# Optimization experiments

Hardware: AMD Instinct MI355X
Metric: run time of the kernel (lower is better)

## Reference

```python
import jax, jax.numpy as jnp
import numpy as np

H = 512; W = 512; WL = 8; SS = 4; DIM = 128; HEADS = 4; HD = DIM // HEADS; HID = 512
N = WL * WL                      # tokens per window = 64
NW = (H // WL) * (W // WL)       # num windows = 4096
EPS = 1e-5


def _rel_pos_index():
    # standard Swin relative position index for a WLxWL window
    coords = np.stack(np.meshgrid(np.arange(WL), np.arange(WL), indexing='ij')).reshape(2, -1)  # [2, N]
    rel = (coords[:, :, None] - coords[:, None, :]).transpose(1, 2, 0)  # [N, N, 2]
    rel[..., 0] += WL - 1
    rel[..., 1] += WL - 1
    rel[..., 0] *= 2 * WL - 1
    return jnp.asarray(rel.sum(-1))  # [N, N] in [0, (2WL-1)^2)


def _shift_attn_mask():
    # region ids 0/1/2 along each axis per the h_slices/w_slices loop, cnt = 3*h_id + w_id
    ids = np.zeros(H)
    ids[H - WL:H - SS] = 1
    ids[H - SS:] = 2
    img = 3.0 * ids[:, None] + ids[None, :]                     # [H, W]
    wnd = img.reshape(H // WL, WL, W // WL, WL).transpose(0, 2, 1, 3).reshape(NW, N)
    diff = wnd[:, None, :] - wnd[:, :, None]                    # [NW, N, N]
    return jnp.asarray(np.where(diff != 0, -100.0, 0.0).astype(np.float32))


REL_IDX = _rel_pos_index()
ATTN_MASK = _shift_attn_mask()


def _layernorm(v, w, b):
    mu = v.mean(-1, keepdims=True)
    var = v.var(-1, keepdims=True)
    return (v - mu) * jax.lax.rsqrt(var + EPS) * w + b


def setup_inputs() -> dict:
    key = jax.random.key(0)
    ks = jax.random.split(key, 10)
    s = 0.02
    return {
        'x': jax.random.normal(ks[0], (H * W, DIM), dtype=jnp.float32),
        'ln1_w': jnp.ones((DIM,), jnp.float32), 'ln1_b': jnp.zeros((DIM,), jnp.float32),
        'qkv_w': jax.random.normal(ks[1], (3 * DIM, DIM), jnp.float32) * s,
        'qkv_b': jnp.zeros((3 * DIM,), jnp.float32),
        'rel_bias': jax.random.normal(ks[2], ((2 * WL - 1) ** 2, HEADS), jnp.float32) * s,
        'proj_w': jax.random.normal(ks[3], (DIM, DIM), jnp.float32) * s,
        'proj_b': jnp.zeros((DIM,), jnp.float32),
        'ln2_w': jnp.ones((DIM,), jnp.float32), 'ln2_b': jnp.zeros((DIM,), jnp.float32),
        'mlp_w1': jax.random.normal(ks[4], (HID, DIM), jnp.float32) * s,
        'mlp_b1': jnp.zeros((HID,), jnp.float32),
        'mlp_w2': jax.random.normal(ks[5], (DIM, HID), jnp.float32) * s,
        'mlp_b2': jnp.zeros((DIM,), jnp.float32),
    }


def reference(x, ln1_w, ln1_b, qkv_w, qkv_b, rel_bias, proj_w, proj_b,
              ln2_w, ln2_b, mlp_w1, mlp_b1, mlp_w2, mlp_b2):
    skip = x
    xn = _layernorm(x, ln1_w, ln1_b).reshape(H, W, DIM)
    # cyclic shift
    xs = jnp.roll(xn, shift=(-SS, -SS), axis=(0, 1))
    # window partition -> [NW, N, DIM]
    xw = xs.reshape(H // WL, WL, W // WL, WL, DIM).transpose(0, 2, 1, 3, 4).reshape(NW, N, DIM)
    # qkv projection, split heads
    qkv = (xw @ qkv_w.T + qkv_b).reshape(NW, N, 3, HEADS, HD)
    q, k, v = qkv[:, :, 0], qkv[:, :, 1], qkv[:, :, 2]   # each [NW, N, HEADS, HD]
    scale = HD ** -0.5
    scores = jnp.einsum('wnhd,wmhd->whnm', q, k) * scale   # [NW, HEADS, N, N]
    bias = rel_bias[REL_IDX].transpose(2, 0, 1)            # [HEADS, N, N]
    scores = scores + bias[None] + ATTN_MASK[:, None]
    attn = jax.nn.softmax(scores, axis=-1)
    out = jnp.einsum('whnm,wmhd->wnhd', attn, v).reshape(NW, N, DIM)
    out = out @ proj_w.T + proj_b
    # window reverse
    xr = out.reshape(H // WL, W // WL, WL, WL, DIM).transpose(0, 2, 1, 3, 4).reshape(H, W, DIM)
    # reverse cyclic shift
    xr = jnp.roll(xr, shift=(SS, SS), axis=(0, 1)).reshape(H * W, DIM)
    x1 = skip + xr
    # FFN block
    h = _layernorm(x1, ln2_w, ln2_b)
    h = jax.nn.gelu(h @ mlp_w1.T + mlp_b1) @ mlp_w2.T + mlp_b2
    return x1 + h
```

## Files before the change

kernel.cpp:

```cpp
#include <hip/hip_runtime.h>
#include <hip/hip_bf16.h>


typedef __bf16 bf16x8 __attribute__((ext_vector_type(8)));
typedef __bf16 bf16x2 __attribute__((ext_vector_type(2)));
typedef float f32x4 __attribute__((ext_vector_type(4)));

#define MFMA16(a, b, c) __builtin_amdgcn_mfma_f32_16x16x32_bf16(a, b, c, 0, 0, 0)

#define SS 4
#define XS 136
#define QKS 40
#define PSS 72

#define QKV_W_OFF 0
#define PROJ_W_OFF 98304
#define W1_OFF 131072
#define W2_OFF 262144
#define BIAS_OFF 393216

__device__ __forceinline__ int regid(int u) { return (u >= 508) ? 2 : ((u >= 504) ? 1 : 0); }

__global__ __launch_bounds__(256) void prep_kernel(
    const float* __restrict__ qkv_w, const float* __restrict__ proj_w,
    const float* __restrict__ w1, const float* __restrict__ w2,
    const float* __restrict__ rel_bias, unsigned char* __restrict__ ws) {
  int tid = blockIdx.x * 256 + threadIdx.x;
  __bf16* qw = (__bf16*)(ws + QKV_W_OFF);
  __bf16* pw = (__bf16*)(ws + PROJ_W_OFF);
  __bf16* w1b = (__bf16*)(ws + W1_OFF);
  __bf16* w2b = (__bf16*)(ws + W2_OFF);
  float* btbl = (float*)(ws + BIAS_OFF);
  if (tid < 49152) {
    int e = tid & 7, lane = (tid >> 3) & 63, kk = (tid >> 9) & 3;
    int f = tid >> 11;
    int h = f / 6, nt = f % 6;
    int j = (nt >> 1) * 128 + h * 32 + (nt & 1) * 16 + (lane & 15);
    int k = kk * 32 + (lane >> 4) * 8 + e;
    qw[tid] = (__bf16)qkv_w[j * 128 + k];
  }
  if (tid < 16384) {
    int e = tid & 7, lane = (tid >> 3) & 63, kk = (tid >> 9) & 3;
    int nt2 = (tid >> 11) & 1, wid = (tid >> 12) & 3;
    int j = wid * 32 + nt2 * 16 + (lane & 15);
    int k = kk * 32 + (lane >> 4) * 8 + e;
    pw[tid] = (__bf16)proj_w[j * 128 + k];
  }
  if (tid < 65536) {
    { int e = tid & 7, lane = (tid >> 3) & 63, kk = (tid >> 9) & 3;
      int nt = (tid >> 11) & 3, wid = (tid >> 13) & 7;
      int j = wid * 64 + nt * 16 + (lane & 15);
      int k = kk * 32 + (lane >> 4) * 8 + e;
      w1b[tid] = (__bf16)w1[j * 128 + k]; }
    { int e = tid & 7, lane = (tid >> 3) & 63, kk = (tid >> 9) & 15, wid = (tid >> 13) & 7;
      int j = wid * 16 + (lane & 15);
      int k = kk * 32 + (lane >> 4) * 8 + e;
      w2b[tid] = (__bf16)w2[j * 512 + k]; }
  }
  if (tid < 16384) {
    int i = tid & 3, lane = (tid >> 2) & 63;
    int kt = (tid >> 8) & 3, qt = (tid >> 10) & 3, h = (tid >> 12) & 3;
    int n = qt * 16 + (lane & 15);
    int m = kt * 16 + (lane >> 4) * 4 + i;
    int idx = ((n >> 3) - (m >> 3) + 7) * 15 + ((n & 7) - (m & 7) + 7);
    btbl[tid] = rel_bias[idx * 4 + h];
  }
}

__global__ __launch_bounds__(256, 2) void attn_kernel(
    const float* __restrict__ x, const float* __restrict__ ln1_w, const float* __restrict__ ln1_b,
    const float* __restrict__ qkv_b, const float* __restrict__ proj_b,
    const unsigned char* __restrict__ ws, float* __restrict__ out) {
  __shared__ __attribute__((aligned(16))) __bf16 xn[64 * XS];
  __shared__ __attribute__((aligned(16))) __bf16 wreg[4][5120];
  __shared__ __attribute__((aligned(16))) __bf16 vt[4][32 * PSS];
  __shared__ __attribute__((aligned(16))) int rid[64];

  const int w = blockIdx.x;
  const int wi = w >> 6, wj = w & 63;
  const int tid = threadIdx.x;
  const int wid = tid >> 6, lane = tid & 63;
  const int lr = lane & 15, lk = lane >> 4;
  const bool edge = (wi == 63) || (wj == 63);
  const f32x4 zero4 = {0.f, 0.f, 0.f, 0.f};

  const __bf16* qw = (const __bf16*)(ws + QKV_W_OFF);
  bf16x8 bw[6][4];
  float qb[6];
#pragma unroll
  for (int nt = 0; nt < 6; nt++) {
    qb[nt] = qkv_b[(nt >> 1) * 128 + wid * 32 + (nt & 1) * 16 + lr];
#pragma unroll
    for (int kk = 0; kk < 4; kk++)
      bw[nt][kk] = *(const bf16x8*)(qw + ((wid * 6 + nt) * 4 + kk) * 512 + lane * 8);
  }

  {
    int n = tid >> 2, q = tid & 3;
    int r = n >> 3, c = n & 7;
    int io = (wi * 8 + r + SS) & 511;
    int jo = (wj * 8 + c + SS) & 511;
    size_t gid = (size_t)io * 512 + jo;
    const float4* xp = (const float4*)(x + gid * 128 + q * 32);
    float4 xv[8];
    float s = 0.f, s2 = 0.f;
#pragma unroll
    for (int t = 0; t < 8; t++) {
      float4 v = xp[t]; xv[t] = v;
      s += v.x + v.y + v.z + v.w;
      s2 += v.x * v.x + v.y * v.y + v.z * v.z + v.w * v.w;
    }
    s += __shfl_xor(s, 1); s += __shfl_xor(s, 2);
    s2 += __shfl_xor(s2, 1); s2 += __shfl_xor(s2, 2);
    float mean = s * (1.f / 128.f);
    float var = s2 * (1.f / 128.f) - mean * mean;
    float rstd = rsqrtf(var + 1e-5f);
    const float4* wv = (const float4*)(ln1_w + q * 32);
    const float4* bv = (const float4*)(ln1_b + q * 32);
    __bf16* dst = xn + n * XS + q * 32;
#pragma unroll
    for (int t = 0; t < 8; t++) {
      float4 wt = wv[t], bt = bv[t], v = xv[t];
      dst[t * 4 + 0] = (__bf16)((v.x - mean) * rstd * wt.x + bt.x);
      dst[t * 4 + 1] = (__bf16)((v.y - mean) * rstd * wt.y + bt.y);
      dst[t * 4 + 2] = (__bf16)((v.z - mean) * rstd * wt.z + bt.z);
      dst[t * 4 + 3] = (__bf16)((v.w - mean) * rstd * wt.w + bt.w);
    }
    if (q == 0) rid[n] = 3 * regid(wi * 8 + r) + regid(wj * 8 + c);
  }
  __syncthreads();

  {
    const float scale = 0.17677669529663687f;
    __bf16* qbase = &wreg[wid][0];
    __bf16* kbase = &wreg[wid][2560];
    __bf16* vbase = &vt[wid][0];
#pragma unroll
    for (int st = 0; st < 4; st++) {
      bf16x8 a[4];
#pragma unroll
      for (int kk = 0; kk < 4; kk++)
        a[kk] = *(const bf16x8*)(xn + (st * 16 + lr) * XS + kk * 32 + lk * 8);
#pragma unroll
      for (int nt = 0; nt < 6; nt++) {
        f32x4 acc = zero4;
#pragma unroll
        for (int kk = 0; kk < 4; kk++) acc = MFMA16(a[kk], bw[nt][kk], acc);
        float bias = qb[nt];
        int dl = (nt & 1) * 16 + lr;
        if (nt < 2) {
#pragma unroll
          for (int i = 0; i < 4; i++)
            qbase[(st * 16 + lk * 4 + i) * QKS + dl] = (__bf16)((acc[i] + bias) * scale);
        } else if (nt < 4) {
#pragma unroll
          for (int i = 0; i < 4; i++)
            kbase[(st * 16 + lk * 4 + i) * QKS + dl] = (__bf16)(acc[i] + bias);
        } else {
#pragma unroll
          for (int i = 0; i < 4; i++)
            vbase[dl * PSS + st * 16 + lk * 4 + i] = (__bf16)(acc[i] + bias);
        }
      }
    }
  }

  const __bf16* pw = (const __bf16*)(ws + PROJ_W_OFF);
  bf16x8 pwf[2][4];
  float pb2[2];
#pragma unroll
  for (int nt2 = 0; nt2 < 2; nt2++) {
    pb2[nt2] = proj_b[wid * 32 + nt2 * 16 + lr];
#pragma unroll
    for (int kk = 0; kk < 4; kk++)
      pwf[nt2][kk] = *(const bf16x8*)(pw + ((wid * 2 + nt2) * 4 + kk) * 512 + lane * 8);
  }
  const float* btbl = (const float*)(ws + BIAS_OFF);
  f32x4 bc[4][4];
#pragma unroll
  for (int qt = 0; qt < 4; qt++)
#pragma unroll
    for (int kt = 0; kt < 4; kt++)
      bc[qt][kt] = *(const f32x4*)(btbl + ((wid * 4 + qt) * 4 + kt) * 256 + lane * 4);

  {
    __bf16* reg0 = &wreg[wid][0];
    bf16x8 kf[4], qf[4], vf[2][2];
#pragma unroll
    for (int kt = 0; kt < 4; kt++)
      kf[kt] = *(const bf16x8*)(reg0 + 2560 + (kt * 16 + lr) * QKS + lk * 8);
#pragma unroll
    for (int qt = 0; qt < 4; qt++)
      qf[qt] = *(const bf16x8*)(reg0 + (qt * 16 + lr) * QKS + lk * 8);
#pragma unroll
    for (int dt = 0; dt < 2; dt++)
#pragma unroll
      for (int kk = 0; kk < 2; kk++)
        vf[dt][kk] = *(const bf16x8*)(&vt[wid][(dt * 16 + lr) * PSS + kk * 32 + lk * 8]);
    asm volatile("s_waitcnt lgkmcnt(0)" ::: "memory");
    __builtin_amdgcn_sched_barrier(0);

    int4 rk[4];
    if (edge) {
#pragma unroll
      for (int kt = 0; kt < 4; kt++) rk[kt] = *(const int4*)&rid[kt * 16 + lk * 4];
    }

#pragma unroll
    for (int qt = 0; qt < 4; qt++) {
      f32x4 s[4];
#pragma unroll
      for (int kt = 0; kt < 4; kt++) s[kt] = MFMA16(kf[kt], qf[qt], bc[qt][kt]);
      if (edge) {
        int rq = rid[qt * 16 + lr];
#pragma unroll
        for (int kt = 0; kt < 4; kt++) {
          s[kt][0] += (rk[kt].x != rq) ? -100.f : 0.f;
          s[kt][1] += (rk[kt].y != rq) ? -100.f : 0.f;
          s[kt][2] += (rk[kt].z != rq) ? -100.f : 0.f;
          s[kt][3] += (rk[kt].w != rq) ? -100.f : 0.f;
        }
      }
      float ex[4][4];
      float sum = 0.f;
#pragma unroll
      for (int kt = 0; kt < 4; kt++) {
#pragma unroll
        for (int i = 0; i < 4; i++) { ex[kt][i] = __expf(s[kt][i]); sum += ex[kt][i]; }
      }
      sum += __shfl_xor(sum, 16);
      sum += __shfl_xor(sum, 32);
      float inv = __builtin_amdgcn_rcpf(sum);
      __bf16* psrow = reg0 + (qt * 16 + lr) * PSS;
#pragma unroll
      for (int kt = 0; kt < 4; kt++) {
        bf16x2 p01 = {(__bf16)(ex[kt][0] * inv), (__bf16)(ex[kt][1] * inv)};
        bf16x2 p23 = {(__bf16)(ex[kt][2] * inv), (__bf16)(ex[kt][3] * inv)};
        *(bf16x2*)(psrow + kt * 16 + lk * 4) = p01;
        *(bf16x2*)(psrow + kt * 16 + lk * 4 + 2) = p23;
      }
#pragma unroll
      for (int dt = 0; dt < 2; dt++) {
        bf16x8 pa0 = *(const bf16x8*)(reg0 + (qt * 16 + lr) * PSS + lk * 8);
        bf16x8 pa1 = *(const bf16x8*)(reg0 + (qt * 16 + lr) * PSS + 32 + lk * 8);
        f32x4 acc = MFMA16(pa0, vf[dt][0], zero4);
        acc = MFMA16(pa1, vf[dt][1], acc);
#pragma unroll
        for (int i = 0; i < 4; i++)
          reg0[qt * 1152 + (lk * 4 + i) * QKS + dt * 16 + lr] = (__bf16)acc[i];
      }
    }
  }
  __syncthreads();

  {
#pragma unroll
    for (int st = 0; st < 4; st++) {
      bf16x8 ao[4];
#pragma unroll
      for (int kk = 0; kk < 4; kk++)
        ao[kk] = *(const bf16x8*)(&wreg[kk][st * 1152 + lr * QKS + lk * 8]);
      size_t gids[4];
#pragma unroll
      for (int i = 0; i < 4; i++) {
        int rr = st * 16 + lk * 4 + i;
        int io = (wi * 8 + (rr >> 3) + SS) & 511;
        int jo = (wj * 8 + (rr & 7) + SS) & 511;
        gids[i] = (size_t)io * 512 + jo;
      }
#pragma unroll
      for (int nt2 = 0; nt2 < 2; nt2++) {
        f32x4 acc = zero4;
#pragma unroll
        for (int kk = 0; kk < 4; kk++) acc = MFMA16(ao[kk], pwf[nt2][kk], acc);
        int j = wid * 32 + nt2 * 16 + lr;
#pragma unroll
        for (int i = 0; i < 4; i++) {
          size_t off = gids[i] * 128 + j;
          out[off] = x[off] + acc[i] + pb2[nt2];
        }
      }
    }
  }
}

__device__ __forceinline__ float gelu_fast(float x) {
  float u = 0.7978845608028654f * x * (1.f + 0.044715f * x * x);
  float e = __expf(2.f * u);
  float th = 1.f - 2.f * __builtin_amdgcn_rcpf(e + 1.f);
  return 0.5f * x * (1.f + th);
}

__global__ __launch_bounds__(512, 1) void mlp_kernel(
    const float* __restrict__ ln2_w, const float* __restrict__ ln2_b,
    const float* __restrict__ mlp_b1, const float* __restrict__ mlp_b2,
    const unsigned char* __restrict__ ws, float* __restrict__ out) {
  __shared__ __attribute__((aligned(16))) __bf16 xn[64 * 128];
  __shared__ __attribute__((aligned(16))) __bf16 hb[64 * 512];
  const int tid = threadIdx.x;
  const int wid = tid >> 6, lane = tid & 63;
  const int lr = lane & 15, lk = lane >> 4;
  const f32x4 zero4 = {0.f, 0.f, 0.f, 0.f};

  const __bf16* w1r = (const __bf16*)(ws + W1_OFF);
  const __bf16* w2r = (const __bf16*)(ws + W2_OFF);
  bf16x8 w1f[4][4], w2f[16];
#pragma unroll
  for (int nt = 0; nt < 4; nt++)
#pragma unroll
    for (int kk = 0; kk < 4; kk++)
      w1f[nt][kk] = *(const bf16x8*)(w1r + ((wid * 4 + nt) * 4 + kk) * 512 + lane * 8);
#pragma unroll
  for (int kk = 0; kk < 16; kk++)
    w2f[kk] = *(const bf16x8*)(w2r + (wid * 16 + kk) * 512 + lane * 8);
  float b1v[4];
#pragma unroll
  for (int nt = 0; nt < 4; nt++) b1v[nt] = mlp_b1[wid * 64 + nt * 16 + lr];
  float b2v = mlp_b2[wid * 16 + lr];

  for (int tt = 0; tt < 4; tt++) {
    const int row0 = (blockIdx.x * 4 + tt) * 64;

    {
      int n = tid >> 3, q = tid & 7;
      const float4* xp = (const float4*)(out + (size_t)(row0 + n) * 128 + q * 16);
      float4 xv[4];
      float s = 0.f, s2 = 0.f;
#pragma unroll
      for (int t = 0; t < 4; t++) {
        float4 v = xp[t]; xv[t] = v;
        s += v.x + v.y + v.z + v.w;
        s2 += v.x * v.x + v.y * v.y + v.z * v.z + v.w * v.w;
      }
      s += __shfl_xor(s, 1); s += __shfl_xor(s, 2); s += __shfl_xor(s, 4);
      s2 += __shfl_xor(s2, 1); s2 += __shfl_xor(s2, 2); s2 += __shfl_xor(s2, 4);
      float mean = s * (1.f / 128.f);
      float var = s2 * (1.f / 128.f) - mean * mean;
      float rstd = rsqrtf(var + 1e-5f);
      const float4* wv = (const float4*)(ln2_w + q * 16);
      const float4* bv = (const float4*)(ln2_b + q * 16);
      bf16x8 o[2];
#pragma unroll
      for (int t = 0; t < 4; t++) {
        float4 wt = wv[t], bt = bv[t], v = xv[t];
        o[t >> 1][(t & 1) * 4 + 0] = (__bf16)((v.x - mean) * rstd * wt.x + bt.x);
        o[t >> 1][(t & 1) * 4 + 1] = (__bf16)((v.y - mean) * rstd * wt.y + bt.y);
        o[t >> 1][(t & 1) * 4 + 2] = (__bf16)((v.z - mean) * rstd * wt.z + bt.z);
        o[t >> 1][(t & 1) * 4 + 3] = (__bf16)((v.w - mean) * rstd * wt.w + bt.w);
      }
      *(bf16x8*)(xn + n * 128 + (((q * 2 + 0) ^ (n & 15)) << 3)) = o[0];
      *(bf16x8*)(xn + n * 128 + (((q * 2 + 1) ^ (n & 15)) << 3)) = o[1];
    }
    __syncthreads();

#pragma unroll 1
    for (int st = 0; st < 4; st++) {
      bf16x8 a1[4];
#pragma unroll
      for (int kk = 0; kk < 4; kk++)
        a1[kk] = *(const bf16x8*)(xn + (st * 16 + lr) * 128 + (((kk * 4 + lk) ^ lr) << 3));
#pragma unroll
      for (int nt = 0; nt < 4; nt++) {
        f32x4 acc = zero4;
#pragma unroll
        for (int kk = 0; kk < 4; kk++) acc = MFMA16(a1[kk], w1f[nt][kk], acc);
        int slot = wid * 8 + nt * 2 + (lr >> 3);
#pragma unroll
        for (int i = 0; i < 4; i++) {
          int row = st * 16 + lk * 4 + i;
          hb[row * 512 + ((slot ^ (row & 15)) << 3) + (lr & 7)] =
              (__bf16)gelu_fast(acc[i] + b1v[nt]);
        }
      }
    }
    __syncthreads();

#pragma unroll 1
    for (int st = 0; st < 4; st++) {
      bf16x8 ah[16];
#pragma unroll
      for (int kk = 0; kk < 16; kk++)
        ah[kk] = *(const bf16x8*)(hb + (st * 16 + lr) * 512 + (((kk * 4 + lk) ^ lr) << 3));
      f32x4 acc0 = zero4, acc1 = zero4;
#pragma unroll
      for (int kk = 0; kk < 8; kk++) {
        acc0 = MFMA16(ah[kk], w2f[kk], acc0);
        acc1 = MFMA16(ah[kk + 8], w2f[kk + 8], acc1);
      }
#pragma unroll
      for (int i = 0; i < 4; i++) {
        size_t off = (size_t)(row0 + st * 16 + lk * 4 + i) * 128 + wid * 16 + lr;
        out[off] = out[off] + acc0[i] + acc1[i] + b2v;
      }
    }
  }
}

extern "C" void kernel_launch(void* const* d_in, const int* in_sizes, int n_in,
                              void* d_out, int out_size, void* d_ws, size_t ws_size,
                              hipStream_t stream) {
  const float* x      = (const float*)d_in[0];
  const float* ln1_w  = (const float*)d_in[1];
  const float* ln1_b  = (const float*)d_in[2];
  const float* qkv_w  = (const float*)d_in[3];
  const float* qkv_b  = (const float*)d_in[4];
  const float* rel_b  = (const float*)d_in[5];
  const float* proj_w = (const float*)d_in[6];
  const float* proj_b = (const float*)d_in[7];
  const float* ln2_w  = (const float*)d_in[8];
  const float* ln2_b  = (const float*)d_in[9];
  const float* mlp_w1 = (const float*)d_in[10];
  const float* mlp_b1 = (const float*)d_in[11];
  const float* mlp_w2 = (const float*)d_in[12];
  const float* mlp_b2 = (const float*)d_in[13];
  float* out = (float*)d_out;
  unsigned char* ws = (unsigned char*)d_ws;

  prep_kernel<<<256, 256, 0, stream>>>(qkv_w, proj_w, mlp_w1, mlp_w2, rel_b, ws);
  attn_kernel<<<4096, 256, 0, stream>>>(x, ln1_w, ln1_b, qkv_b, proj_b, ws, out);
  mlp_kernel<<<1024, 512, 0, stream>>>(ln2_w, ln2_b, mlp_b1, mlp_b2, ws, out);
}
```

Baseline: 260.6 us.

## Prefetch residual and next-tile inputs early, replace syncthreads with LDS-only barriers

The attention kernel now loads the residual x values into registers before the attention compute, so their global latency overlaps with the math instead of stalling the final projection store. The MLP kernel prefetches the next 64-row tile of out while the current tile's MFMAs run, and streams the hidden-layer A fragments per k-step instead of loading all 16 up front. Several __syncthreads are replaced with an lgkmcnt(0) wait plus s_barrier, so outstanding global loads no longer have to drain at each barrier. The cost is higher register pressure: 32 extra floats for the residual and 16 for the prefetch, which could spill or lower occupancy.

```diff
diff --git a/kernel.cpp b/kernel.cpp
--- a/kernel.cpp
+++ b/kernel.cpp
@@ -7,6 +7,9 @@
 typedef float f32x4 __attribute__((ext_vector_type(4)));
 
 #define MFMA16(a, b, c) __builtin_amdgcn_mfma_f32_16x16x32_bf16(a, b, c, 0, 0, 0)
+#define LGKM_BARRIER() do { \
+    asm volatile("s_waitcnt lgkmcnt(0)" ::: "memory"); \
+    __builtin_amdgcn_s_barrier(); } while (0)
 
 #define SS 4
 #define XS 136
@@ -128,7 +131,7 @@
     }
     if (q == 0) rid[n] = 3 * regid(wi * 8 + r) + regid(wj * 8 + c);
   }
-  __syncthreads();
+  LGKM_BARRIER();
 
   {
     const float scale = 0.17677669529663687f;
@@ -182,6 +185,25 @@
 #pragma unroll
     for (int kt = 0; kt < 4; kt++)
       bc[qt][kt] = *(const f32x4*)(btbl + ((wid * 4 + qt) * 4 + kt) * 256 + lane * 4);
+
+  int gidx[4][4];
+#pragma unroll
+  for (int st = 0; st < 4; st++)
+#pragma unroll
+    for (int i = 0; i < 4; i++) {
+      int rr = st * 16 + lk * 4 + i;
+      int io = (wi * 8 + (rr >> 3) + SS) & 511;
+      int jo = (wj * 8 + (rr & 7) + SS) & 511;
+      gidx[st][i] = io * 512 + jo;
+    }
+  float xres[4][2][4];
+#pragma unroll
+  for (int st = 0; st < 4; st++)
+#pragma unroll
+    for (int nt2 = 0; nt2 < 2; nt2++)
+#pragma unroll
+      for (int i = 0; i < 4; i++)
+        xres[st][nt2][i] = x[(size_t)gidx[st][i] * 128 + wid * 32 + nt2 * 16 + lr];
 
   {
     __bf16* reg0 = &wreg[wid][0];
@@ -251,7 +273,7 @@
       }
     }
   }
-  __syncthreads();
+  LGKM_BARRIER();
 
   {
 #pragma unroll
@@ -260,14 +282,6 @@
 #pragma unroll
       for (int kk = 0; kk < 4; kk++)
         ao[kk] = *(const bf16x8*)(&wreg[kk][st * 1152 + lr * QKS + lk * 8]);
-      size_t gids[4];
-#pragma unroll
-      for (int i = 0; i < 4; i++) {
-        int rr = st * 16 + lk * 4 + i;
-        int io = (wi * 8 + (rr >> 3) + SS) & 511;
-        int jo = (wj * 8 + (rr & 7) + SS) & 511;
-        gids[i] = (size_t)io * 512 + jo;
-      }
 #pragma unroll
       for (int nt2 = 0; nt2 < 2; nt2++) {
         f32x4 acc = zero4;
@@ -276,8 +290,8 @@
         int j = wid * 32 + nt2 * 16 + lr;
 #pragma unroll
         for (int i = 0; i < 4; i++) {
-          size_t off = gids[i] * 128 + j;
-          out[off] = x[off] + acc[i] + pb2[nt2];
+          size_t off = (size_t)gidx[st][i] * 128 + j;
+          out[off] = xres[st][nt2][i] + acc[i] + pb2[nt2];
         }
       }
     }
@@ -318,17 +332,22 @@
   for (int nt = 0; nt < 4; nt++) b1v[nt] = mlp_b1[wid * 64 + nt * 16 + lr];
   float b2v = mlp_b2[wid * 16 + lr];
 
+  const int n = tid >> 3, q = tid & 7;
+  float4 xv[4];
+  {
+    const float4* xp = (const float4*)(out + (size_t)(blockIdx.x * 256 + n) * 128 + q * 16);
+#pragma unroll
+    for (int t = 0; t < 4; t++) xv[t] = xp[t];
+  }
+
   for (int tt = 0; tt < 4; tt++) {
     const int row0 = (blockIdx.x * 4 + tt) * 64;
 
     {
-      int n = tid >> 3, q = tid & 7;
-      const float4* xp = (const float4*)(out + (size_t)(row0 + n) * 128 + q * 16);
-      float4 xv[4];
       float s = 0.f, s2 = 0.f;
 #pragma unroll
       for (int t = 0; t < 4; t++) {
-        float4 v = xp[t]; xv[t] = v;
+        float4 v = xv[t];
         s += v.x + v.y + v.z + v.w;
         s2 += v.x * v.x + v.y * v.y + v.z * v.z + v.w * v.w;
       }
@@ -351,7 +370,12 @@
       *(bf16x8*)(xn + n * 128 + (((q * 2 + 0) ^ (n & 15)) << 3)) = o[0];
       *(bf16x8*)(xn + n * 128 + (((q * 2 + 1) ^ (n & 15)) << 3)) = o[1];
     }
-    __syncthreads();
+    if (tt < 3) {
+      const float4* xp = (const float4*)(out + (size_t)(row0 + 64 + n) * 128 + q * 16);
+#pragma unroll
+      for (int t = 0; t < 4; t++) xv[t] = xp[t];
+    }
+    LGKM_BARRIER();
 
 #pragma unroll 1
     for (int st = 0; st < 4; st++) {
@@ -373,19 +397,17 @@
         }
       }
     }
-    __syncthreads();
+    LGKM_BARRIER();
 
 #pragma unroll 1
     for (int st = 0; st < 4; st++) {
-      bf16x8 ah[16];
-#pragma unroll
-      for (int kk = 0; kk < 16; kk++)
-        ah[kk] = *(const bf16x8*)(hb + (st * 16 + lr) * 512 + (((kk * 4 + lk) ^ lr) << 3));
       f32x4 acc0 = zero4, acc1 = zero4;
 #pragma unroll
       for (int kk = 0; kk < 8; kk++) {
-        acc0 = MFMA16(ah[kk], w2f[kk], acc0);
-        acc1 = MFMA16(ah[kk + 8], w2f[kk + 8], acc1);
+        bf16x8 a0 = *(const bf16x8*)(hb + (st * 16 + lr) * 512 + (((kk * 4 + lk) ^ lr) << 3));
+        bf16x8 a1h = *(const bf16x8*)(hb + (st * 16 + lr) * 512 + ((((kk + 8) * 4 + lk) ^ lr) << 3));
+        acc0 = MFMA16(a0, w2f[kk], acc0);
+        acc1 = MFMA16(a1h, w2f[kk + 8], acc1);
       }
 #pragma unroll
       for (int i = 0; i < 4; i++) {
```

After: 291.8 us. +11.9%, slower.
